# Kernel tuning notes

Hardware: AMD Instinct MI355X
Metric: run time of the kernel (lower is better)

Reference implementation:

```python
import jax, jax.numpy as jnp
import numpy as np

N_NODES = 50000      # batch of nodes
N_UNIQUE = 100000    # rows in pre_hidden_embs
K = 16               # sampled neighbors per node
IN_DIM = 128
OUT_DIM = 128


def setup_inputs() -> dict:
    key = jax.random.key(0)
    k1, k2, k3, k4 = jax.random.split(key, 4)
    nodes = jax.random.randint(k1, (N_NODES,), 0, N_UNIQUE)
    pre_hidden_embs = jax.random.normal(k2, (N_UNIQUE, IN_DIM), dtype=jnp.float32)
    neigh_idx = jax.random.randint(k3, (N_NODES, K), 0, N_UNIQUE)
    # xavier-uniform-like init for weight (out_dim, in_dim*2)
    fan_in, fan_out = 2 * IN_DIM, OUT_DIM
    bound = np.sqrt(6.0 / (fan_in + fan_out))
    weight = jax.random.uniform(k4, (OUT_DIM, 2 * IN_DIM), dtype=jnp.float32,
                                minval=-bound, maxval=bound)
    return {"nodes": nodes, "pre_hidden_embs": pre_hidden_embs,
            "neigh_idx": neigh_idx, "weight": weight}


def reference(nodes, pre_hidden_embs, neigh_idx, weight):
    # message(): dense row-normalized mask mm == mean over sampled neighbors
    # [N, K, D] gather then mean -> [N, D]
    aggregate_feats = jnp.mean(pre_hidden_embs[neigh_idx], axis=1)
    # self features
    self_feats = pre_hidden_embs[nodes]                       # [N, D]
    # update(): concat -> relu(W @ combined.T).T == relu(combined @ W.T)
    combined = jnp.concatenate([self_feats, aggregate_feats], axis=1)  # [N, 2D]
    out_emb = jax.nn.relu(combined @ weight.T)                # [N, OUT_DIM]
    return out_emb
```

## Files before the change

kernel.cpp:

```cpp
#include <hip/hip_runtime.h>

#define K_NEIGH 16
#define IN_DIM 128
#define OUT_DIM 128
#define TWO_D 256

#define BM 16
#define LSTR 264

typedef __attribute__((ext_vector_type(8))) short bf16x8;
typedef __attribute__((ext_vector_type(4))) unsigned short u16x4;
typedef __attribute__((ext_vector_type(4))) float f32x4;
typedef __attribute__((ext_vector_type(2))) float f32x2;

__device__ __forceinline__ unsigned short f2bf(float x) {
    union { float f; unsigned u; } v; v.f = x;
    unsigned r = v.u + 0x7fffu + ((v.u >> 16) & 1u);
    return (unsigned short)(r >> 16);
}

__global__ void prep_all(const float* __restrict__ W, const float* __restrict__ embs,
                         unsigned short* __restrict__ wfrag, unsigned* __restrict__ f8tab,
                         int total_ints) {
    const int b = blockIdx.x;
    if (b < 16) {
        const int t = b * 256 + threadIdx.x;
        const int lane = t & 63;
        const int ks = (t >> 6) & 7;
        const int nt = t >> 9;
        const int n  = nt * 16 + (lane & 15);
        const int k0 = ks * 32 + (lane >> 4) * 8;
        const float* src = W + (size_t)n * TWO_D + k0;
        const float4 a = *reinterpret_cast<const float4*>(src);
        const float4 c = *reinterpret_cast<const float4*>(src + 4);
        ushort4 lo = { f2bf(a.x), f2bf(a.y), f2bf(a.z), f2bf(a.w) };
        ushort4 hi = { f2bf(c.x), f2bf(c.y), f2bf(c.z), f2bf(c.w) };
        unsigned short* dst = wfrag + (size_t)t * 8;
        *reinterpret_cast<ushort4*>(dst)     = lo;
        *reinterpret_cast<ushort4*>(dst + 4) = hi;
    } else {
        int i = (b - 16) * 256 + threadIdx.x;
        const int stride = (gridDim.x - 16) * 256;
        for (; i < total_ints; i += stride) {
            const float4 v = reinterpret_cast<const float4*>(embs)[i];
            int p = 0;
            p = __builtin_amdgcn_cvt_pk_fp8_f32(v.x, v.y, p, false);
            p = __builtin_amdgcn_cvt_pk_fp8_f32(v.z, v.w, p, true);
            f8tab[i] = (unsigned)p;
        }
    }
}

template <int USE_F8>
__global__ __launch_bounds__(512, 8)
void sage_fused(const int* __restrict__ nodes,
                const float* __restrict__ embs,
                const unsigned* __restrict__ f8tab,
                const int* __restrict__ neigh,
                const unsigned short* __restrict__ wfrag,
                float* __restrict__ out,
                int n_nodes)
{
    __shared__ unsigned short comb[BM * LSTR];
    __shared__ int sidx[BM];
    __shared__ int nb[BM * K_NEIGH];

    const int tid = threadIdx.x;
    const int block_n0 = blockIdx.x * BM;
    const int nvalid = min(BM, n_nodes - block_n0);

    if (tid < BM)
        sidx[tid] = (tid < nvalid) ? nodes[block_n0 + tid] : 0;
    if (tid < BM * K_NEIGH)
        nb[tid] = (tid < nvalid * K_NEIGH) ? neigh[(size_t)block_n0 * K_NEIGH + tid] : 0;
    __syncthreads();

    {
        const int nloc = tid >> 5;
        const int l = tid & 31;
        unsigned short* row = &comb[nloc * LSTR];
        if (nloc < nvalid) {
            const int* nptr = &nb[nloc * K_NEIGH];
            const float4 sv = *reinterpret_cast<const float4*>(
                embs + (size_t)sidx[nloc] * IN_DIM + 4 * l);
            ushort4 t4 = { f2bf(sv.x), f2bf(sv.y), f2bf(sv.z), f2bf(sv.w) };
            *reinterpret_cast<ushort4*>(row + 4 * l) = t4;

            float ax[4] = {0.f, 0.f, 0.f, 0.f};
            if (USE_F8) {
                unsigned v[K_NEIGH];
                #pragma unroll
                for (int k = 0; k < K_NEIGH; ++k)
                    v[k] = f8tab[(size_t)nptr[k] * (IN_DIM / 4) + l];
                #pragma unroll
                for (int k = 0; k < K_NEIGH; ++k) {
                    const f32x2 lo = __builtin_amdgcn_cvt_pk_f32_fp8((int)v[k], false);
                    const f32x2 hi = __builtin_amdgcn_cvt_pk_f32_fp8((int)v[k], true);
                    ax[0] += lo[0]; ax[1] += lo[1]; ax[2] += hi[0]; ax[3] += hi[1];
                }
            } else {
                #pragma unroll
                for (int b2 = 0; b2 < 2; ++b2) {
                    float4 v[8];
                    #pragma unroll
                    for (int k = 0; k < 8; ++k)
                        v[k] = *reinterpret_cast<const float4*>(
                            embs + (size_t)nptr[b2 * 8 + k] * IN_DIM + 4 * l);
                    #pragma unroll
                    for (int k = 0; k < 8; ++k) {
                        ax[0] += v[k].x; ax[1] += v[k].y; ax[2] += v[k].z; ax[3] += v[k].w;
                    }
                }
            }
            u16x4 m4;
            #pragma unroll
            for (int j = 0; j < 4; ++j) m4[j] = f2bf(ax[j] * 0.0625f);
            *reinterpret_cast<u16x4*>(row + IN_DIM + 4 * l) = m4;
        } else {
            u16x4 z = { 0, 0, 0, 0 };
            *reinterpret_cast<u16x4*>(row + 4 * l) = z;
            *reinterpret_cast<u16x4*>(row + IN_DIM + 4 * l) = z;
        }
    }
    __syncthreads();

    const int wave = tid >> 6;
    const int lane = tid & 63;
    const int row16 = lane & 15;
    const int hi    = lane >> 4;

    f32x4 acc = {0, 0, 0, 0};
    {
        const unsigned short* arow = &comb[row16 * LSTR + hi * 8];
        const unsigned short* bbase = wfrag + ((size_t)wave * 8 * 64 + (size_t)lane) * 8;
        #pragma unroll
        for (int ks = 0; ks < 8; ++ks) {
            const bf16x8 a = *reinterpret_cast<const bf16x8*>(arow + ks * 32);
            const bf16x8 b = *reinterpret_cast<const bf16x8*>(bbase + (size_t)ks * 64 * 8);
            acc = __builtin_amdgcn_mfma_f32_16x16x32_bf16(a, b, acc, 0, 0, 0);
        }
    }
    __syncthreads();

    {
        float* otile = reinterpret_cast<float*>(comb);
        const int ncol = wave * 16 + row16;
        #pragma unroll
        for (int r = 0; r < 4; ++r)
            otile[(hi * 4 + r) * 132 + ncol] = fmaxf(acc[r], 0.f);
        __syncthreads();

        const int rrow = tid >> 5;
        const int seg  = tid & 31;
        if (rrow < nvalid) {
            *reinterpret_cast<float4*>(out + (size_t)(block_n0 + rrow) * OUT_DIM + seg * 4) =
                *reinterpret_cast<const float4*>(otile + rrow * 132 + seg * 4);
        }
    }
}

extern "C" void kernel_launch(void* const* d_in, const int* in_sizes, int n_in,
                              void* d_out, int out_size, void* d_ws, size_t ws_size,
                              hipStream_t stream) {
    const int*   nodes = (const int*)d_in[0];
    const float* embs  = (const float*)d_in[1];
    const int*   neigh = (const int*)d_in[2];
    const float* W     = (const float*)d_in[3];
    float* out = (float*)d_out;

    const int n_nodes = in_sizes[0];
    const int n_unique = in_sizes[1] / IN_DIM;
    const size_t f8tab_bytes = (size_t)n_unique * IN_DIM;
    const size_t wfrag_bytes = 8 * 8 * 64 * 8 * 2;
    const bool use_f8 = ws_size >= f8tab_bytes + wfrag_bytes;

    unsigned char* base = (unsigned char*)d_ws;
    unsigned* f8tab = (unsigned*)base;
    unsigned short* wfrag = (unsigned short*)(use_f8 ? base + f8tab_bytes : base);

    const int grid = (n_nodes + BM - 1) / BM;

    if (use_f8) {
        const int total_ints = (int)(f8tab_bytes / 4);
        prep_all<<<16 + 2048, 256, 0, stream>>>(W, embs, wfrag, f8tab, total_ints);
        sage_fused<1><<<grid, 512, 0, stream>>>(nodes, embs, f8tab, neigh, wfrag, out, n_nodes);
    } else {
        prep_all<<<16, 256, 0, stream>>>(W, embs, wfrag, f8tab, 0);
        sage_fused<0><<<grid, 512, 0, stream>>>(nodes, embs, f8tab, neigh, wfrag, out, n_nodes);
    }
}
```

Baseline: 40.21 us.

## Double rows per block with two-pass gather and 2x1 MFMA tiling

The node tile per block grows from 16 to 32 rows, so each thread gathers two nodes in sequence. The MFMA stage is remapped so each wave computes two 16x16 output tiles that share one A fragment, which halves weight-fragment reuse traffic per row. Output stores become two nontemporal 16-byte stores per thread. The aim is to amortise block setup and weight loads over more rows. The cost is fewer blocks, more shared memory per block, and possibly lower occupancy and less latency hiding for the gather.

Result: slower. 42.48 us (+5.6%).

```diff
diff --git a/kernel.cpp b/kernel.cpp
--- a/kernel.cpp
+++ b/kernel.cpp
@@ -5,7 +5,7 @@
 #define OUT_DIM 128
 #define TWO_D 256
 
-#define BM 16
+#define BM 32
 #define LSTR 264
 
 typedef __attribute__((ext_vector_type(8))) short bf16x8;
@@ -71,55 +71,57 @@
 
     if (tid < BM)
         sidx[tid] = (tid < nvalid) ? nodes[block_n0 + tid] : 0;
-    if (tid < BM * K_NEIGH)
-        nb[tid] = (tid < nvalid * K_NEIGH) ? neigh[(size_t)block_n0 * K_NEIGH + tid] : 0;
+    nb[tid] = (tid < nvalid * K_NEIGH) ? neigh[(size_t)block_n0 * K_NEIGH + tid] : 0;
     __syncthreads();
 
     {
-        const int nloc = tid >> 5;
         const int l = tid & 31;
-        unsigned short* row = &comb[nloc * LSTR];
-        if (nloc < nvalid) {
-            const int* nptr = &nb[nloc * K_NEIGH];
-            const float4 sv = *reinterpret_cast<const float4*>(
-                embs + (size_t)sidx[nloc] * IN_DIM + 4 * l);
-            ushort4 t4 = { f2bf(sv.x), f2bf(sv.y), f2bf(sv.z), f2bf(sv.w) };
-            *reinterpret_cast<ushort4*>(row + 4 * l) = t4;
-
-            float ax[4] = {0.f, 0.f, 0.f, 0.f};
-            if (USE_F8) {
-                unsigned v[K_NEIGH];
-                #pragma unroll
-                for (int k = 0; k < K_NEIGH; ++k)
-                    v[k] = f8tab[(size_t)nptr[k] * (IN_DIM / 4) + l];
-                #pragma unroll
-                for (int k = 0; k < K_NEIGH; ++k) {
-                    const f32x2 lo = __builtin_amdgcn_cvt_pk_f32_fp8((int)v[k], false);
-                    const f32x2 hi = __builtin_amdgcn_cvt_pk_f32_fp8((int)v[k], true);
-                    ax[0] += lo[0]; ax[1] += lo[1]; ax[2] += hi[0]; ax[3] += hi[1];
-                }
-            } else {
-                #pragma unroll
-                for (int b2 = 0; b2 < 2; ++b2) {
-                    float4 v[8];
+        #pragma unroll
+        for (int s = 0; s < 2; ++s) {
+            const int nloc = s * 16 + (tid >> 5);
+            unsigned short* row = &comb[nloc * LSTR];
+            if (nloc < nvalid) {
+                const int* nptr = &nb[nloc * K_NEIGH];
+                const float4 sv = *reinterpret_cast<const float4*>(
+                    embs + (size_t)sidx[nloc] * IN_DIM + 4 * l);
+
+                float ax[4] = {0.f, 0.f, 0.f, 0.f};
+                if (USE_F8) {
+                    unsigned v[K_NEIGH];
                     #pragma unroll
-                    for (int k = 0; k < 8; ++k)
-                        v[k] = *reinterpret_cast<const float4*>(
-                            embs + (size_t)nptr[b2 * 8 + k] * IN_DIM + 4 * l);
+                    for (int k = 0; k < K_NEIGH; ++k)
+                        v[k] = f8tab[(size_t)nptr[k] * (IN_DIM / 4) + l];
                     #pragma unroll
-                    for (int k = 0; k < 8; ++k) {
-                        ax[0] += v[k].x; ax[1] += v[k].y; ax[2] += v[k].z; ax[3] += v[k].w;
+                    for (int k = 0; k < K_NEIGH; ++k) {
+                        const f32x2 lo = __builtin_amdgcn_cvt_pk_f32_fp8((int)v[k], false);
+                        const f32x2 hi = __builtin_amdgcn_cvt_pk_f32_fp8((int)v[k], true);
+                        ax[0] += lo[0]; ax[1] += lo[1]; ax[2] += hi[0]; ax[3] += hi[1];
+                    }
+                } else {
+                    #pragma unroll
+                    for (int b2 = 0; b2 < 2; ++b2) {
+                        float4 v[8];
+                        #pragma unroll
+                        for (int k = 0; k < 8; ++k)
+                            v[k] = *reinterpret_cast<const float4*>(
+                                embs + (size_t)nptr[b2 * 8 + k] * IN_DIM + 4 * l);
+                        #pragma unroll
+                        for (int k = 0; k < 8; ++k) {
+                            ax[0] += v[k].x; ax[1] += v[k].y; ax[2] += v[k].z; ax[3] += v[k].w;
+                        }
                     }
                 }
+                ushort4 t4 = { f2bf(sv.x), f2bf(sv.y), f2bf(sv.z), f2bf(sv.w) };
+                *reinterpret_cast<ushort4*>(row + 4 * l) = t4;
+                u16x4 m4;
+                #pragma unroll
+                for (int j = 0; j < 4; ++j) m4[j] = f2bf(ax[j] * 0.0625f);
+                *reinterpret_cast<u16x4*>(row + IN_DIM + 4 * l) = m4;
+            } else {
+                u16x4 z = { 0, 0, 0, 0 };
+                *reinterpret_cast<u16x4*>(row + 4 * l) = z;
+                *reinterpret_cast<u16x4*>(row + IN_DIM + 4 * l) = z;
             }
-            u16x4 m4;
-            #pragma unroll
-            for (int j = 0; j < 4; ++j) m4[j] = f2bf(ax[j] * 0.0625f);
-            *reinterpret_cast<u16x4*>(row + IN_DIM + 4 * l) = m4;
-        } else {
-            u16x4 z = { 0, 0, 0, 0 };
-            *reinterpret_cast<u16x4*>(row + 4 * l) = z;
-            *reinterpret_cast<u16x4*>(row + IN_DIM + 4 * l) = z;
         }
     }
     __syncthreads();
@@ -128,33 +130,43 @@
     const int lane = tid & 63;
     const int row16 = lane & 15;
     const int hi    = lane >> 4;
-
-    f32x4 acc = {0, 0, 0, 0};
+    const int mt = wave & 1;
+    const int nq0 = wave >> 1;
+
+    f32x4 acc0 = {0,0,0,0}, acc1 = {0,0,0,0};
     {
-        const unsigned short* arow = &comb[row16 * LSTR + hi * 8];
-        const unsigned short* bbase = wfrag + ((size_t)wave * 8 * 64 + (size_t)lane) * 8;
+        const unsigned short* arow = &comb[(mt * 16 + row16) * LSTR + hi * 8];
+        const unsigned short* bb0 = wfrag + ((size_t)nq0 * 8 * 64 + (size_t)lane) * 8;
+        const unsigned short* bb1 = wfrag + ((size_t)(nq0 + 4) * 8 * 64 + (size_t)lane) * 8;
         #pragma unroll
         for (int ks = 0; ks < 8; ++ks) {
-            const bf16x8 a = *reinterpret_cast<const bf16x8*>(arow + ks * 32);
-            const bf16x8 b = *reinterpret_cast<const bf16x8*>(bbase + (size_t)ks * 64 * 8);
-            acc = __builtin_amdgcn_mfma_f32_16x16x32_bf16(a, b, acc, 0, 0, 0);
+            const bf16x8 a  = *reinterpret_cast<const bf16x8*>(arow + ks * 32);
+            const bf16x8 b0 = *reinterpret_cast<const bf16x8*>(bb0 + (size_t)ks * 64 * 8);
+            const bf16x8 b1 = *reinterpret_cast<const bf16x8*>(bb1 + (size_t)ks * 64 * 8);
+            acc0 = __builtin_amdgcn_mfma_f32_16x16x32_bf16(a, b0, acc0, 0, 0, 0);
+            acc1 = __builtin_amdgcn_mfma_f32_16x16x32_bf16(a, b1, acc1, 0, 0, 0);
         }
     }
     __syncthreads();
 
     {
         float* otile = reinterpret_cast<float*>(comb);
-        const int ncol = wave * 16 + row16;
         #pragma unroll
-        for (int r = 0; r < 4; ++r)
-            otile[(hi * 4 + r) * 132 + ncol] = fmaxf(acc[r], 0.f);
+        for (int r = 0; r < 4; ++r) {
+            const int mrow = mt * 16 + hi * 4 + r;
+            otile[mrow * 132 + nq0 * 16 + row16]       = fmaxf(acc0[r], 0.f);
+            otile[mrow * 132 + (nq0 + 4) * 16 + row16] = fmaxf(acc1[r], 0.f);
+        }
         __syncthreads();
 
-        const int rrow = tid >> 5;
-        const int seg  = tid & 31;
+        const int rrow = tid >> 4;
+        const int seg  = tid & 15;
         if (rrow < nvalid) {
-            *reinterpret_cast<float4*>(out + (size_t)(block_n0 + rrow) * OUT_DIM + seg * 4) =
-                *reinterpret_cast<const float4*>(otile + rrow * 132 + seg * 4);
+            const f32x4* src = reinterpret_cast<const f32x4*>(otile + rrow * 132 + seg * 8);
+            f32x4* dst = reinterpret_cast<f32x4*>(
+                out + (size_t)(block_n0 + rrow) * OUT_DIM + seg * 8);
+            __builtin_nontemporal_store(src[0], dst);
+            __builtin_nontemporal_store(src[1], dst + 1);
         }
     }
 }
```
